# Performance work log

Hardware: AMD Instinct MI355X
Metric: run time of the kernel (lower is better)

## Reference

```python
import jax, jax.numpy as jnp
import numpy as np

B, N, DIM = 2, 2048, 1024
H, DH = 16, 64
INNER = H * DH
SCALE = DH ** -0.5


def rotate_half(x):
    x1, x2 = jnp.split(x, 2, axis=-1)
    return jnp.concatenate((-x2, x1), axis=-1)


def apply_rotary(pos, t):
    # pos: [n, dh] broadcast against t: [b, h, n, dh]
    return t * jnp.cos(pos) + rotate_half(t) * jnp.sin(pos)


def setup_inputs() -> dict:
    key = jax.random.key(0)
    ks = jax.random.split(key, 5)
    x = jax.random.normal(ks[0], (B, N, DIM), dtype=jnp.float32)
    rotary_emb = jax.random.normal(ks[1], (N, DH), dtype=jnp.float32)
    w_qkv = jax.random.normal(ks[2], (3 * INNER, DIM), dtype=jnp.float32) * (DIM ** -0.5)
    w_out = jax.random.normal(ks[3], (DIM, INNER), dtype=jnp.float32) * (INNER ** -0.5)
    b_out = jax.random.normal(ks[4], (DIM,), dtype=jnp.float32) * 0.01
    return {"x": x, "rotary_emb": rotary_emb, "w_qkv": w_qkv, "w_out": w_out, "b_out": b_out}


def reference(x, rotary_emb, w_qkv, w_out, b_out):
    b, n, _ = x.shape
    qkv = jnp.einsum('bnd,ed->bne', x, w_qkv)  # [b, n, 3*inner]
    q, k, v = jnp.split(qkv, 3, axis=-1)
    # [b, n, inner] -> [b, h, n, dh]
    reshape = lambda t: t.reshape(b, n, H, DH).transpose(0, 2, 1, 3)
    q, k, v = reshape(q), reshape(k), reshape(v)
    q = apply_rotary(rotary_emb, q)
    k = apply_rotary(rotary_emb, k)
    dots = jnp.einsum('bhid,bhjd->bhij', q, k) * SCALE
    attn = jax.nn.softmax(dots, axis=-1)
    out = jnp.einsum('bhij,bhjd->bhid', attn, v)
    out = out.transpose(0, 2, 1, 3).reshape(b, n, INNER)
    return jnp.einsum('bne,de->bnd', out, w_out) + b_out
```

## Files before the change

kernel.cpp:

```cpp
#include <hip/hip_runtime.h>
#include <math.h>

typedef unsigned short ushort_t;
typedef __attribute__((ext_vector_type(8))) short short8v;
typedef __attribute__((ext_vector_type(4))) float float4v;

#define BB 2
#define NN 2048
#define HH 16
#define DHH 64
#define DIMM 1024
#define QKV3 3072
#define INNERR 1024
#define QSCALE 0.1803368801111244f

__device__ __forceinline__ ushort_t f2bf(float f) {
    unsigned u = __float_as_uint(f);
    u += 0x7fffu + ((u >> 16) & 1u);
    return (ushort_t)(u >> 16);
}
__device__ __forceinline__ float bf2f(unsigned h) {
    return __uint_as_float(h << 16);
}
__device__ __forceinline__ unsigned pk_bf16(float a, float b) {
#if __has_builtin(__builtin_amdgcn_cvt_pk_bf16_f32)
    typedef __attribute__((ext_vector_type(2))) __bf16 bf16x2;
    bf16x2 r = __builtin_amdgcn_cvt_pk_bf16_f32(a, b);
    return __builtin_bit_cast(unsigned, r);
#else
    return (unsigned)f2bf(a) | ((unsigned)f2bf(b) << 16);
#endif
}
__device__ __forceinline__ float fast_exp2(float x) {
#if __has_builtin(__builtin_amdgcn_exp2f)
    return __builtin_amdgcn_exp2f(x);
#else
    return exp2f(x);
#endif
}
__device__ __forceinline__ float fast_rcp(float x) {
#if __has_builtin(__builtin_amdgcn_rcpf)
    return __builtin_amdgcn_rcpf(x);
#else
    return 1.0f / x;
#endif
}
__device__ __forceinline__ void gl2lds16(const void* g, void* l) {
    __builtin_amdgcn_global_load_lds(
        (const __attribute__((address_space(1))) unsigned int*)g,
        (__attribute__((address_space(3))) unsigned int*)l, 16, 0, 0);
}

__global__ __launch_bounds__(256) void conv_fused(const float* __restrict__ x,
                                                  const float* __restrict__ wqkv,
                                                  const float* __restrict__ wout,
                                                  ushort_t* __restrict__ xo,
                                                  ushort_t* __restrict__ wqkvo,
                                                  ushort_t* __restrict__ wouto) {
    int blk = blockIdx.x;
    const float* in; ushort_t* out; int i;
    if (blk < 4096)      { in = x;    out = xo;    i = blk * 256 + threadIdx.x; }
    else if (blk < 7168) { in = wqkv; out = wqkvo; i = (blk - 4096) * 256 + threadIdx.x; }
    else                 { in = wout; out = wouto; i = (blk - 7168) * 256 + threadIdx.x; }
    float4 v = ((const float4*)in)[i];
    ushort4 o;
    o.x = f2bf(v.x); o.y = f2bf(v.y); o.z = f2bf(v.z); o.w = f2bf(v.w);
    ((ushort4*)out)[i] = o;
}

template <int NOUT, bool BF16OUT, bool BIAS, bool ROT>
__global__ __launch_bounds__(256, 3) void gemm128(const ushort_t* __restrict__ A,
                                                  const ushort_t* __restrict__ Bm,
                                                  const float* __restrict__ bias,
                                                  const float* __restrict__ rot,
                                                  ushort_t* __restrict__ Vt,
                                                  void* __restrict__ Cout, int K) {
    constexpr int NCH = 4;
    __shared__ ushort_t As[2][128 * 32];
    __shared__ ushort_t Bs[2][128 * 32];
    const int t = threadIdx.x;
    const int lane = t & 63;
    const int w = t >> 6;
    const int wr = w >> 1;
    const int wc = w & 1;
    const int quad = lane >> 4;
    const int l15 = lane & 15;
    const int m0 = blockIdx.y * 128;
    const int n0 = blockIdx.x * 128;

    float4v acc[4][4];
#pragma unroll
    for (int i = 0; i < 4; ++i)
#pragma unroll
        for (int j = 0; j < 4; ++j) acc[i][j] = (float4v)0.0f;

    int srow[NCH], slc[NCH], sdst[NCH];
    bool sisA[NCH];
#pragma unroll
    for (int u = 0; u < NCH; ++u) {
        int c = u * 256 + t;
        if (c < 512) {
            int row = c >> 2;
            sisA[u] = true; srow[u] = row; slc[u] = (c & 3) ^ ((row >> 1) & 3); sdst[u] = c * 8;
        } else {
            int cb = c - 512;
            int row = cb >> 2;
            sisA[u] = false; srow[u] = row; slc[u] = (cb & 3) ^ ((row >> 1) & 3); sdst[u] = cb * 8;
        }
    }
#pragma unroll
    for (int u = 0; u < NCH; ++u) {
        if (sisA[u]) gl2lds16(&A[(size_t)(m0 + srow[u]) * K + slc[u] * 8], &As[0][sdst[u]]);
        else         gl2lds16(&Bm[(size_t)(n0 + srow[u]) * K + slc[u] * 8], &Bs[0][sdst[u]]);
    }
    const int NIT = K >> 5;
    for (int it = 0; it < NIT; ++it) {
        const int cur = it & 1;
        if (it + 1 < NIT) {
            const int nxt = cur ^ 1;
            const int kc = (it + 1) << 5;
#pragma unroll
            for (int u = 0; u < NCH; ++u) {
                if (sisA[u]) gl2lds16(&A[(size_t)(m0 + srow[u]) * K + kc + slc[u] * 8], &As[nxt][sdst[u]]);
                else         gl2lds16(&Bm[(size_t)(n0 + srow[u]) * K + kc + slc[u] * 8], &Bs[nxt][sdst[u]]);
            }
            asm volatile("s_waitcnt vmcnt(4)\n\ts_barrier" ::: "memory");
        } else {
            asm volatile("s_waitcnt vmcnt(0)\n\ts_barrier" ::: "memory");
        }
        short8v a[4], b[4];
#pragma unroll
        for (int i = 0; i < 4; ++i) {
            int row = wr * 64 + i * 16 + l15;
            int pc = quad ^ ((row >> 1) & 3);
            a[i] = *(const short8v*)&As[cur][row * 32 + pc * 8];
        }
#pragma unroll
        for (int j = 0; j < 4; ++j) {
            int row = wc * 64 + j * 16 + l15;
            int pc = quad ^ ((row >> 1) & 3);
            b[j] = *(const short8v*)&Bs[cur][row * 32 + pc * 8];
        }
#pragma unroll
        for (int i = 0; i < 4; ++i)
#pragma unroll
            for (int j = 0; j < 4; ++j)
                acc[i][j] = __builtin_amdgcn_mfma_f32_16x16x32_bf16(a[i], b[j], acc[i][j], 0, 0, 0);
        asm volatile("s_barrier" ::: "memory");
    }
    const int region = ROT ? (n0 >> 10) : 0;
    if (ROT && region == 2) {
#pragma unroll
        for (int i = 0; i < 4; ++i) {
            int grow = m0 + wr * 64 + i * 16 + quad * 4;
            int bb = grow >> 11, nn_ = grow & (NN - 1);
            int tk = nn_ & 63;
            int tp = (tk & 32) | ((tk & 12) << 1) | ((tk & 16) >> 2);
            int nstore = (nn_ & ~63) | tp;
#pragma unroll
            for (int j = 0; j < 4; ++j) {
                int vcol = n0 + wc * 64 + j * 16 + l15 - 2048;
                int hh = vcol >> 6, dh = vcol & 63;
                uint2 st;
                st.x = pk_bf16(acc[i][j][0], acc[i][j][1]);
                st.y = pk_bf16(acc[i][j][2], acc[i][j][3]);
                *(uint2*)&Vt[((size_t)(bb * HH + hh) * DHH + dh) * NN + nstore] = st;
            }
        }
        return;
    }
    if (ROT) {
        float scale = (region == 0) ? QSCALE : 1.0f;
#pragma unroll
        for (int i = 0; i < 4; ++i) {
#pragma unroll
            for (int r = 0; r < 4; ++r) {
                int n = (m0 + wr * 64 + i * 16 + quad * 4 + r) & (NN - 1);
#pragma unroll
                for (int jl = 0; jl < 2; ++jl) {
                    int dh = jl * 16 + l15;
                    float plo = rot[n * DHH + dh];
                    float phi = rot[n * DHH + dh + 32];
                    float lo = acc[i][jl][r], hi = acc[i][jl + 2][r];
                    acc[i][jl][r]     = (lo * __cosf(plo) - hi * __sinf(plo)) * scale;
                    acc[i][jl + 2][r] = (hi * __cosf(phi) + lo * __sinf(phi)) * scale;
                }
            }
        }
    }
#pragma unroll
    for (int i = 0; i < 4; ++i) {
        int grow = m0 + wr * 64 + i * 16 + quad * 4;
#pragma unroll
        for (int j = 0; j < 4; ++j) {
            int gcol = n0 + wc * 64 + j * 16 + l15;
            float bv = BIAS ? bias[gcol] : 0.0f;
#pragma unroll
            for (int r = 0; r < 4; ++r) {
                float v = acc[i][j][r] + bv;
                if (BF16OUT)
                    ((ushort_t*)Cout)[(size_t)(grow + r) * NOUT + gcol] = f2bf(v);
                else
                    ((float*)Cout)[(size_t)(grow + r) * NOUT + gcol] = v;
            }
        }
    }
}

template <int NOUT, bool BIAS>
__global__ __launch_bounds__(256, 3) void gemm_bk64(const ushort_t* __restrict__ A,
                                                    const ushort_t* __restrict__ Bm,
                                                    const float* __restrict__ bias,
                                                    float* __restrict__ Cout, int K) {
    __shared__ ushort_t As[2][128 * 64];
    __shared__ ushort_t Bs[2][64 * 64];
    const int t = threadIdx.x;
    const int lane = t & 63;
    const int w = t >> 6;
    const int wr = w >> 1;
    const int wc = w & 1;
    const int quad = lane >> 4;
    const int l15 = lane & 15;
    const int m0 = blockIdx.y * 128;
    const int n0 = blockIdx.x * 64;

    float4v acc[4][2];
#pragma unroll
    for (int i = 0; i < 4; ++i)
#pragma unroll
        for (int j = 0; j < 2; ++j) acc[i][j] = (float4v)0.0f;

    int row_[6], lcv[6], dst[6];
#pragma unroll
    for (int u = 0; u < 6; ++u) {
        int c = u * 256 + t;
        int cb = (u < 4) ? c : (c - 1024);
        int row = cb >> 3;
        row_[u] = row;
        lcv[u] = (cb & 7) ^ (row & 7);
        dst[u] = cb * 8;
    }
#pragma unroll
    for (int u = 0; u < 6; ++u) {
        if (u < 4) gl2lds16(&A[(size_t)(m0 + row_[u]) * K + lcv[u] * 8], &As[0][dst[u]]);
        else       gl2lds16(&Bm[(size_t)(n0 + row_[u]) * K + lcv[u] * 8], &Bs[0][dst[u]]);
    }
    const int NIT = K >> 6;
    for (int it = 0; it < NIT; ++it) {
        const int cur = it & 1;
        if (it + 1 < NIT) {
            const int nxt = cur ^ 1;
            const int kc = (it + 1) << 6;
#pragma unroll
            for (int u = 0; u < 6; ++u) {
                if (u < 4) gl2lds16(&A[(size_t)(m0 + row_[u]) * K + kc + lcv[u] * 8], &As[nxt][dst[u]]);
                else       gl2lds16(&Bm[(size_t)(n0 + row_[u]) * K + kc + lcv[u] * 8], &Bs[nxt][dst[u]]);
            }
            asm volatile("s_waitcnt vmcnt(6)\n\ts_barrier" ::: "memory");
        } else {
            asm volatile("s_waitcnt vmcnt(0)\n\ts_barrier" ::: "memory");
        }
        short8v a[2][4], b[2][2];
#pragma unroll
        for (int i = 0; i < 4; ++i) {
            int row = wr * 64 + i * 16 + l15;
            int r7 = row & 7;
            a[0][i] = *(const short8v*)&As[cur][row * 64 + ((quad) ^ r7) * 8];
            a[1][i] = *(const short8v*)&As[cur][row * 64 + ((4 + quad) ^ r7) * 8];
        }
#pragma unroll
        for (int j = 0; j < 2; ++j) {
            int row = wc * 32 + j * 16 + l15;
            int r7 = row & 7;
            b[0][j] = *(const short8v*)&Bs[cur][row * 64 + ((quad) ^ r7) * 8];
            b[1][j] = *(const short8v*)&Bs[cur][row * 64 + ((4 + quad) ^ r7) * 8];
        }
#pragma unroll
        for (int kh = 0; kh < 2; ++kh)
#pragma unroll
            for (int i = 0; i < 4; ++i)
#pragma unroll
                for (int j = 0; j < 2; ++j)
                    acc[i][j] = __builtin_amdgcn_mfma_f32_16x16x32_bf16(a[kh][i], b[kh][j], acc[i][j], 0, 0, 0);
        asm volatile("s_barrier" ::: "memory");
    }
#pragma unroll
    for (int i = 0; i < 4; ++i) {
        int grow = m0 + wr * 64 + i * 16 + quad * 4;
#pragma unroll
        for (int j = 0; j < 2; ++j) {
            int gcol = n0 + wc * 32 + j * 16 + l15;
            float bv = BIAS ? bias[gcol] : 0.0f;
#pragma unroll
            for (int r = 0; r < 4; ++r)
                Cout[(size_t)(grow + r) * NOUT + gcol] = acc[i][j][r] + bv;
        }
    }
}

__global__ __launch_bounds__(256, 2) void flash_mfma(const ushort_t* __restrict__ qkv,
                                                     const ushort_t* __restrict__ Vt,
                                                     ushort_t* __restrict__ attn) {
    __shared__ ushort_t smem[16384];
    const int t = threadIdx.x;
    const int lane = t & 63;
    const int w = t >> 6;
    const int quad = lane >> 4;
    const int l15 = lane & 15;
    const int blk = blockIdx.x;
    const int slot = blk >> 3;
    const int qt = slot & 15;
    const int bh = (blk & 7) * 4 + (slot >> 4);
    const int b = bh >> 4, h = bh & 15;
    const int n0 = qt * 128;

    short8v bq[2][2];
#pragma unroll
    for (int g = 0; g < 2; ++g) {
        size_t qb = (size_t)(b * NN + n0 + w * 32 + g * 16 + l15) * QKV3 + h * DHH + quad * 8;
        bq[g][0] = *(const short8v*)&qkv[qb];
        bq[g][1] = *(const short8v*)&qkv[qb + 32];
    }
    float4v o_acc[2][4];
    float4v l_acc[2];
#pragma unroll
    for (int g = 0; g < 2; ++g) {
        l_acc[g] = (float4v)0.0f;
#pragma unroll
        for (int nb = 0; nb < 4; ++nb) o_acc[g][nb] = (float4v)0.0f;
    }
    const short one_bf = (short)0x3F80;
    short8v ones8 = {one_bf, one_bf, one_bf, one_bf, one_bf, one_bf, one_bf, one_bf};
    const float4v ZR = (float4v)0.0f;

    const int s0 = t, s1 = 256 + t;
    const int r0 = s0 >> 3, lc0 = (s0 & 7) ^ (r0 & 7);
    const int r1 = s1 >> 3, lc1 = (s1 & 7) ^ (r1 & 7);
    const int koff0 = r0 * QKV3 + lc0 * 8, koff1 = r1 * QKV3 + lc1 * 8;
    const int voff0 = r0 * NN + lc0 * 8,   voff1 = r1 * NN + lc1 * 8;
    const ushort_t* kp = qkv + (size_t)b * NN * QKV3 + INNERR + h * DHH;
    const ushort_t* vp = Vt + (size_t)(b * HH + h) * DHH * NN;

    {
        gl2lds16(kp + koff0, smem + 0 * 4096 + s0 * 8);
        gl2lds16(kp + koff1, smem + 0 * 4096 + s1 * 8);
        gl2lds16(vp + voff0, smem + 2 * 4096 + s0 * 8);
        gl2lds16(vp + voff1, smem + 2 * 4096 + s1 * 8);
    }
    for (int jt = 0; jt < 32; ++jt) {
        const int cur = jt & 1;
        if (jt < 31) {
            kp += 64 * QKV3;
            vp += 64;
            const int nxt = cur ^ 1;
            gl2lds16(kp + koff0, smem + nxt * 4096 + s0 * 8);
            gl2lds16(kp + koff1, smem + nxt * 4096 + s1 * 8);
            gl2lds16(vp + voff0, smem + (2 + nxt) * 4096 + s0 * 8);
            gl2lds16(vp + voff1, smem + (2 + nxt) * 4096 + s1 * 8);
            asm volatile("s_waitcnt vmcnt(4)\n\ts_barrier" ::: "memory");
        } else {
            asm volatile("s_waitcnt vmcnt(0)\n\ts_barrier" ::: "memory");
        }
        const ushort_t* Ksc = smem + cur * 4096;
        const ushort_t* Vtc = smem + (2 + cur) * 4096;
        short8v ak[2][4], bv[2][4];
#pragma unroll
        for (int nb = 0; nb < 4; ++nb) {
            int row = nb * 16 + l15;
            int base = row * 64;
            int r7 = row & 7;
            ak[0][nb] = *(const short8v*)&Ksc[base + ((quad) ^ r7) * 8];
            ak[1][nb] = *(const short8v*)&Ksc[base + ((4 + quad) ^ r7) * 8];
            bv[0][nb] = *(const short8v*)&Vtc[base + ((quad) ^ r7) * 8];
            bv[1][nb] = *(const short8v*)&Vtc[base + ((4 + quad) ^ r7) * 8];
        }
        __builtin_amdgcn_s_setprio(1);
        float4v s0v[4], s1v[4];
#pragma unroll
        for (int nb = 0; nb < 4; ++nb)
            s0v[nb] = __builtin_amdgcn_mfma_f32_16x16x32_bf16(ak[0][nb], bq[0][0], ZR, 0, 0, 0);
#pragma unroll
        for (int nb = 0; nb < 4; ++nb)
            s0v[nb] = __builtin_amdgcn_mfma_f32_16x16x32_bf16(ak[1][nb], bq[0][1], s0v[nb], 0, 0, 0);
#pragma unroll
        for (int nb = 0; nb < 4; ++nb)
            s1v[nb] = __builtin_amdgcn_mfma_f32_16x16x32_bf16(ak[0][nb], bq[1][0], ZR, 0, 0, 0);
#pragma unroll
        for (int nb = 0; nb < 4; ++nb)
            s1v[nb] = __builtin_amdgcn_mfma_f32_16x16x32_bf16(ak[1][nb], bq[1][1], s1v[nb], 0, 0, 0);
#pragma unroll
        for (int g = 0; g < 2; ++g) {
            float4v* sv = (g == 0) ? s0v : s1v;
            float p[4][4];
#pragma unroll
            for (int nb = 0; nb < 4; ++nb)
#pragma unroll
                for (int r = 0; r < 4; ++r) p[nb][r] = fast_exp2(sv[nb][r]);
            uint4 u0, u1;
            u0.x = pk_bf16(p[0][0], p[0][1]); u0.y = pk_bf16(p[0][2], p[0][3]);
            u0.z = pk_bf16(p[1][0], p[1][1]); u0.w = pk_bf16(p[1][2], p[1][3]);
            u1.x = pk_bf16(p[2][0], p[2][1]); u1.y = pk_bf16(p[2][2], p[2][3]);
            u1.z = pk_bf16(p[3][0], p[3][1]); u1.w = pk_bf16(p[3][2], p[3][3]);
            short8v ap0 = __builtin_bit_cast(short8v, u0);
            short8v ap1 = __builtin_bit_cast(short8v, u1);
            l_acc[g] = __builtin_amdgcn_mfma_f32_16x16x32_bf16(ap0, ones8, l_acc[g], 0, 0, 0);
            l_acc[g] = __builtin_amdgcn_mfma_f32_16x16x32_bf16(ap1, ones8, l_acc[g], 0, 0, 0);
#pragma unroll
            for (int nb = 0; nb < 4; ++nb) {
                o_acc[g][nb] = __builtin_amdgcn_mfma_f32_16x16x32_bf16(ap0, bv[0][nb], o_acc[g][nb], 0, 0, 0);
                o_acc[g][nb] = __builtin_amdgcn_mfma_f32_16x16x32_bf16(ap1, bv[1][nb], o_acc[g][nb], 0, 0, 0);
            }
        }
        __builtin_amdgcn_s_setprio(0);
        asm volatile("s_barrier" ::: "memory");
    }
    float inv[2][4];
#pragma unroll
    for (int g = 0; g < 2; ++g)
#pragma unroll
        for (int r = 0; r < 4; ++r) inv[g][r] = fast_rcp(l_acc[g][r]);
    ushort_t* osc = smem + w * (32 * 68);
#pragma unroll
    for (int g = 0; g < 2; ++g)
#pragma unroll
        for (int nb = 0; nb < 4; ++nb)
#pragma unroll
            for (int r = 0; r < 4; ++r)
                osc[(g * 16 + quad * 4 + r) * 68 + nb * 16 + l15] = f2bf(o_acc[g][nb][r] * inv[g][r]);
    __builtin_amdgcn_s_waitcnt(0);
    {
        int rr = lane >> 1, c0 = (lane & 1) * 32;
        size_t arow = ((size_t)(b * NN + n0 + w * 32 + rr)) * INNERR + h * DHH + c0;
#pragma unroll
        for (int u = 0; u < 4; ++u) {
            uint4 v = *(const uint4*)&osc[rr * 68 + c0 + u * 8];
            *(uint4*)&attn[arow + u * 8] = v;
        }
    }
}

extern "C" void kernel_launch(void* const* d_in, const int* in_sizes, int n_in,
                              void* d_out, int out_size, void* d_ws, size_t ws_size,
                              hipStream_t stream) {
    const float* x = (const float*)d_in[0];
    const float* rot = (const float*)d_in[1];
    const float* w_qkv = (const float*)d_in[2];
    const float* w_out = (const float*)d_in[3];
    const float* b_out = (const float*)d_in[4];
    float* y = (float*)d_out;

    char* ws = (char*)d_ws;
    ushort_t* qkv_bf  = (ushort_t*)(ws);
    ushort_t* vt_bf   = (ushort_t*)(ws + 25165824);
    ushort_t* wout_bf = (ushort_t*)(ws + 33554432);
    ushort_t* wqkv_bf = (ushort_t*)(ws + 35651584);
    ushort_t* x_bf    = (ushort_t*)(ws + 41943040);
    ushort_t* attn_bf = x_bf;

    conv_fused<<<8192, 256, 0, stream>>>(x, w_qkv, w_out, x_bf, wqkv_bf, wout_bf);
    gemm128<QKV3, true, false, true><<<dim3(24, 32), 256, 0, stream>>>(
        x_bf, wqkv_bf, nullptr, rot, vt_bf, qkv_bf, DIMM);
    flash_mfma<<<512, 256, 0, stream>>>(qkv_bf, vt_bf, attn_bf);
    gemm_bk64<INNERR, true><<<dim3(16, 32), 256, 0, stream>>>(
        attn_bf, wout_bf, b_out, y, INNERR);
}
```

Before: 177.4 us.

## Fuse x fp32-to-bf16 conversion into QKV GEMM loads; shrink output GEMM tile

```diff
diff --git a/kernel.cpp b/kernel.cpp
--- a/kernel.cpp
+++ b/kernel.cpp
@@ -51,32 +51,26 @@
         (__attribute__((address_space(3))) unsigned int*)l, 16, 0, 0);
 }
 
-__global__ __launch_bounds__(256) void conv_fused(const float* __restrict__ x,
-                                                  const float* __restrict__ wqkv,
+__global__ __launch_bounds__(256) void conv_fused(const float* __restrict__ wqkv,
                                                   const float* __restrict__ wout,
-                                                  ushort_t* __restrict__ xo,
                                                   ushort_t* __restrict__ wqkvo,
                                                   ushort_t* __restrict__ wouto) {
     int blk = blockIdx.x;
     const float* in; ushort_t* out; int i;
-    if (blk < 4096)      { in = x;    out = xo;    i = blk * 256 + threadIdx.x; }
-    else if (blk < 7168) { in = wqkv; out = wqkvo; i = (blk - 4096) * 256 + threadIdx.x; }
-    else                 { in = wout; out = wouto; i = (blk - 7168) * 256 + threadIdx.x; }
+    if (blk < 3072) { in = wqkv; out = wqkvo; i = blk * 256 + threadIdx.x; }
+    else            { in = wout; out = wouto; i = (blk - 3072) * 256 + threadIdx.x; }
     float4 v = ((const float4*)in)[i];
     ushort4 o;
     o.x = f2bf(v.x); o.y = f2bf(v.y); o.z = f2bf(v.z); o.w = f2bf(v.w);
     ((ushort4*)out)[i] = o;
 }
 
-template <int NOUT, bool BF16OUT, bool BIAS, bool ROT>
-__global__ __launch_bounds__(256, 3) void gemm128(const ushort_t* __restrict__ A,
-                                                  const ushort_t* __restrict__ Bm,
-                                                  const float* __restrict__ bias,
-                                                  const float* __restrict__ rot,
-                                                  ushort_t* __restrict__ Vt,
-                                                  void* __restrict__ Cout, int K) {
-    constexpr int NCH = 4;
-    __shared__ ushort_t As[2][128 * 32];
+__global__ __launch_bounds__(256, 3) void gemm1_rot(const float* __restrict__ Ax,
+                                                    const ushort_t* __restrict__ Bm,
+                                                    const float* __restrict__ rot,
+                                                    ushort_t* __restrict__ Vt,
+                                                    ushort_t* __restrict__ Cout, int K) {
+    __shared__ float    Asf[2][128 * 32];
     __shared__ ushort_t Bs[2][128 * 32];
     const int t = threadIdx.x;
     const int lane = t & 63;
@@ -94,24 +88,27 @@
 #pragma unroll
         for (int j = 0; j < 4; ++j) acc[i][j] = (float4v)0.0f;
 
-    int srow[NCH], slc[NCH], sdst[NCH];
-    bool sisA[NCH];
-#pragma unroll
-    for (int u = 0; u < NCH; ++u) {
+    int row_[6], lcv[6], dst[6];
+#pragma unroll
+    for (int u = 0; u < 6; ++u) {
         int c = u * 256 + t;
-        if (c < 512) {
-            int row = c >> 2;
-            sisA[u] = true; srow[u] = row; slc[u] = (c & 3) ^ ((row >> 1) & 3); sdst[u] = c * 8;
+        if (u < 4) {
+            int row = c >> 3;
+            row_[u] = row;
+            lcv[u] = (c & 7) ^ (row & 7);
+            dst[u] = c * 4;
         } else {
-            int cb = c - 512;
+            int cb = c - 1024;
             int row = cb >> 2;
-            sisA[u] = false; srow[u] = row; slc[u] = (cb & 3) ^ ((row >> 1) & 3); sdst[u] = cb * 8;
-        }
-    }
-#pragma unroll
-    for (int u = 0; u < NCH; ++u) {
-        if (sisA[u]) gl2lds16(&A[(size_t)(m0 + srow[u]) * K + slc[u] * 8], &As[0][sdst[u]]);
-        else         gl2lds16(&Bm[(size_t)(n0 + srow[u]) * K + slc[u] * 8], &Bs[0][sdst[u]]);
+            row_[u] = row;
+            lcv[u] = (cb & 3) ^ ((row >> 1) & 3);
+            dst[u] = cb * 8;
+        }
+    }
+#pragma unroll
+    for (int u = 0; u < 6; ++u) {
+        if (u < 4) gl2lds16(&Ax[(size_t)(m0 + row_[u]) * K + lcv[u] * 4], &Asf[0][dst[u]]);
+        else       gl2lds16(&Bm[(size_t)(n0 + row_[u]) * K + lcv[u] * 8], &Bs[0][dst[u]]);
     }
     const int NIT = K >> 5;
     for (int it = 0; it < NIT; ++it) {
@@ -120,11 +117,11 @@
             const int nxt = cur ^ 1;
             const int kc = (it + 1) << 5;
 #pragma unroll
-            for (int u = 0; u < NCH; ++u) {
-                if (sisA[u]) gl2lds16(&A[(size_t)(m0 + srow[u]) * K + kc + slc[u] * 8], &As[nxt][sdst[u]]);
-                else         gl2lds16(&Bm[(size_t)(n0 + srow[u]) * K + kc + slc[u] * 8], &Bs[nxt][sdst[u]]);
+            for (int u = 0; u < 6; ++u) {
+                if (u < 4) gl2lds16(&Ax[(size_t)(m0 + row_[u]) * K + kc + lcv[u] * 4], &Asf[nxt][dst[u]]);
+                else       gl2lds16(&Bm[(size_t)(n0 + row_[u]) * K + kc + lcv[u] * 8], &Bs[nxt][dst[u]]);
             }
-            asm volatile("s_waitcnt vmcnt(4)\n\ts_barrier" ::: "memory");
+            asm volatile("s_waitcnt vmcnt(6)\n\ts_barrier" ::: "memory");
         } else {
             asm volatile("s_waitcnt vmcnt(0)\n\ts_barrier" ::: "memory");
         }
@@ -132,8 +129,13 @@
 #pragma unroll
         for (int i = 0; i < 4; ++i) {
             int row = wr * 64 + i * 16 + l15;
-            int pc = quad ^ ((row >> 1) & 3);
-            a[i] = *(const short8v*)&As[cur][row * 32 + pc * 8];
+            int r7 = row & 7;
+            float4v raw0 = *(const float4v*)&Asf[cur][row * 32 + ((2 * quad) ^ r7) * 4];
+            float4v raw1 = *(const float4v*)&Asf[cur][row * 32 + ((2 * quad + 1) ^ r7) * 4];
+            uint4 u_;
+            u_.x = pk_bf16(raw0[0], raw0[1]); u_.y = pk_bf16(raw0[2], raw0[3]);
+            u_.z = pk_bf16(raw1[0], raw1[1]); u_.w = pk_bf16(raw1[2], raw1[3]);
+            a[i] = __builtin_bit_cast(short8v, u_);
         }
 #pragma unroll
         for (int j = 0; j < 4; ++j) {
@@ -148,8 +150,8 @@
                 acc[i][j] = __builtin_amdgcn_mfma_f32_16x16x32_bf16(a[i], b[j], acc[i][j], 0, 0, 0);
         asm volatile("s_barrier" ::: "memory");
     }
-    const int region = ROT ? (n0 >> 10) : 0;
-    if (ROT && region == 2) {
+    const int region = n0 >> 10;
+    if (region == 2) {
 #pragma unroll
         for (int i = 0; i < 4; ++i) {
             int grow = m0 + wr * 64 + i * 16 + quad * 4;
@@ -169,7 +171,7 @@
         }
         return;
     }
-    if (ROT) {
+    {
         float scale = (region == 0) ? QSCALE : 1.0f;
 #pragma unroll
         for (int i = 0; i < 4; ++i) {
@@ -194,25 +196,19 @@
 #pragma unroll
         for (int j = 0; j < 4; ++j) {
             int gcol = n0 + wc * 64 + j * 16 + l15;
-            float bv = BIAS ? bias[gcol] : 0.0f;
-#pragma unroll
-            for (int r = 0; r < 4; ++r) {
-                float v = acc[i][j][r] + bv;
-                if (BF16OUT)
-                    ((ushort_t*)Cout)[(size_t)(grow + r) * NOUT + gcol] = f2bf(v);
-                else
-                    ((float*)Cout)[(size_t)(grow + r) * NOUT + gcol] = v;
-            }
+#pragma unroll
+            for (int r = 0; r < 4; ++r)
+                Cout[(size_t)(grow + r) * QKV3 + gcol] = f2bf(acc[i][j][r]);
         }
     }
 }
 
 template <int NOUT, bool BIAS>
-__global__ __launch_bounds__(256, 3) void gemm_bk64(const ushort_t* __restrict__ A,
-                                                    const ushort_t* __restrict__ Bm,
-                                                    const float* __restrict__ bias,
-                                                    float* __restrict__ Cout, int K) {
-    __shared__ ushort_t As[2][128 * 64];
+__global__ __launch_bounds__(256, 4) void gemm_64(const ushort_t* __restrict__ A,
+                                                  const ushort_t* __restrict__ Bm,
+                                                  const float* __restrict__ bias,
+                                                  float* __restrict__ Cout, int K) {
+    __shared__ ushort_t As[2][64 * 64];
     __shared__ ushort_t Bs[2][64 * 64];
     const int t = threadIdx.x;
     const int lane = t & 63;
@@ -221,28 +217,28 @@
     const int wc = w & 1;
     const int quad = lane >> 4;
     const int l15 = lane & 15;
-    const int m0 = blockIdx.y * 128;
+    const int m0 = blockIdx.y * 64;
     const int n0 = blockIdx.x * 64;
 
-    float4v acc[4][2];
-#pragma unroll
-    for (int i = 0; i < 4; ++i)
+    float4v acc[2][2];
+#pragma unroll
+    for (int i = 0; i < 2; ++i)
 #pragma unroll
         for (int j = 0; j < 2; ++j) acc[i][j] = (float4v)0.0f;
 
-    int row_[6], lcv[6], dst[6];
-#pragma unroll
-    for (int u = 0; u < 6; ++u) {
+    int row_[4], lcv[4], dst[4];
+#pragma unroll
+    for (int u = 0; u < 4; ++u) {
         int c = u * 256 + t;
-        int cb = (u < 4) ? c : (c - 1024);
+        int cb = (u < 2) ? c : (c - 512);
         int row = cb >> 3;
         row_[u] = row;
         lcv[u] = (cb & 7) ^ (row & 7);
         dst[u] = cb * 8;
     }
 #pragma unroll
-    for (int u = 0; u < 6; ++u) {
-        if (u < 4) gl2lds16(&A[(size_t)(m0 + row_[u]) * K + lcv[u] * 8], &As[0][dst[u]]);
+    for (int u = 0; u < 4; ++u) {
+        if (u < 2) gl2lds16(&A[(size_t)(m0 + row_[u]) * K + lcv[u] * 8], &As[0][dst[u]]);
         else       gl2lds16(&Bm[(size_t)(n0 + row_[u]) * K + lcv[u] * 8], &Bs[0][dst[u]]);
     }
     const int NIT = K >> 6;
@@ -252,18 +248,18 @@
             const int nxt = cur ^ 1;
             const int kc = (it + 1) << 6;
 #pragma unroll
-            for (int u = 0; u < 6; ++u) {
-                if (u < 4) gl2lds16(&A[(size_t)(m0 + row_[u]) * K + kc + lcv[u] * 8], &As[nxt][dst[u]]);
+            for (int u = 0; u < 4; ++u) {
+                if (u < 2) gl2lds16(&A[(size_t)(m0 + row_[u]) * K + kc + lcv[u] * 8], &As[nxt][dst[u]]);
                 else       gl2lds16(&Bm[(size_t)(n0 + row_[u]) * K + kc + lcv[u] * 8], &Bs[nxt][dst[u]]);
             }
-            asm volatile("s_waitcnt vmcnt(6)\n\ts_barrier" ::: "memory");
+            asm volatile("s_waitcnt vmcnt(4)\n\ts_barrier" ::: "memory");
         } else {
             asm volatile("s_waitcnt vmcnt(0)\n\ts_barrier" ::: "memory");
         }
-        short8v a[2][4], b[2][2];
-#pragma unroll
-        for (int i = 0; i < 4; ++i) {
-            int row = wr * 64 + i * 16 + l15;
+        short8v a[2][2], b[2][2];
+#pragma unroll
+        for (int i = 0; i < 2; ++i) {
+            int row = wr * 32 + i * 16 + l15;
             int r7 = row & 7;
             a[0][i] = *(const short8v*)&As[cur][row * 64 + ((quad) ^ r7) * 8];
             a[1][i] = *(const short8v*)&As[cur][row * 64 + ((4 + quad) ^ r7) * 8];
@@ -278,15 +274,15 @@
 #pragma unroll
         for (int kh = 0; kh < 2; ++kh)
 #pragma unroll
-            for (int i = 0; i < 4; ++i)
+            for (int i = 0; i < 2; ++i)
 #pragma unroll
                 for (int j = 0; j < 2; ++j)
                     acc[i][j] = __builtin_amdgcn_mfma_f32_16x16x32_bf16(a[kh][i], b[kh][j], acc[i][j], 0, 0, 0);
         asm volatile("s_barrier" ::: "memory");
     }
 #pragma unroll
-    for (int i = 0; i < 4; ++i) {
-        int grow = m0 + wr * 64 + i * 16 + quad * 4;
+    for (int i = 0; i < 2; ++i) {
+        int grow = m0 + wr * 32 + i * 16 + quad * 4;
 #pragma unroll
         for (int j = 0; j < 2; ++j) {
             int gcol = n0 + wc * 32 + j * 16 + l15;
@@ -454,13 +450,12 @@
     ushort_t* vt_bf   = (ushort_t*)(ws + 25165824);
     ushort_t* wout_bf = (ushort_t*)(ws + 33554432);
     ushort_t* wqkv_bf = (ushort_t*)(ws + 35651584);
-    ushort_t* x_bf    = (ushort_t*)(ws + 41943040);
-    ushort_t* attn_bf = x_bf;
-
-    conv_fused<<<8192, 256, 0, stream>>>(x, w_qkv, w_out, x_bf, wqkv_bf, wout_bf);
-    gemm128<QKV3, true, false, true><<<dim3(24, 32), 256, 0, stream>>>(
-        x_bf, wqkv_bf, nullptr, rot, vt_bf, qkv_bf, DIMM);
+    ushort_t* attn_bf = (ushort_t*)(ws + 41943040);
+
+    conv_fused<<<4096, 256, 0, stream>>>(w_qkv, w_out, wqkv_bf, wout_bf);
+    gemm1_rot<<<dim3(24, 32), 256, 0, stream>>>(
+        x, wqkv_bf, rot, vt_bf, qkv_bf, DIMM);
     flash_mfma<<<512, 256, 0, stream>>>(qkv_bf, vt_bf, attn_bf);
-    gemm_bk64<INNERR, true><<<dim3(16, 32), 256, 0, stream>>>(
+    gemm_64<INNERR, true><<<dim3(16, 64), 256, 0, stream>>>(
         attn_bf, wout_bf, b_out, y, INNERR);
 }
```

After: 183.8 us. 1.04x slower.
